# Optimization experiments

Measured on AMD Instinct MI355X. Metric: run time of the kernel, lower is better.

Reference implementation:

```python
import jax, jax.numpy as jnp
import numpy as np

B, S, K = 8, 512, 16  # batch, image size, max highlight points per image
EMPTY_DIST = 362.1    # sentinel used by the torch code when no highlights exist

SOBEL = jnp.array([
    [[[-1.0, 0.0, 1.0], [-2.0, 0.0, 2.0], [-1.0, 0.0, 1.0]]],
    [[[ 1.0, 2.0, 1.0], [ 0.0, 0.0, 0.0], [-1.0, -2.0, -1.0]]],
    [[[ 2.0, 1.0, 0.0], [ 1.0, 0.0, -1.0], [ 0.0, -1.0, -2.0]]],
    [[[ 0.0, 1.0, 2.0], [-1.0, 0.0, 1.0], [-2.0, -1.0, 0.0]]],
], dtype=jnp.float32)  # [4,1,3,3] OIHW


def setup_inputs() -> dict:
    key = jax.random.key(0)
    k1, k2, k3 = jax.random.split(key, 3)
    pred = jax.random.uniform(k1, (B, 1, S, S), dtype=jnp.float32)
    ori_img = jax.random.uniform(k2, (B, 1, S, S), dtype=jnp.float32)
    # sparse point labels: K random highlight pixels per image
    coords = jax.random.randint(k3, (B, K, 2), 0, S)
    b_idx = jnp.repeat(jnp.arange(B), K)
    pt_label = jnp.zeros((B, 1, S, S), dtype=jnp.float32).at[
        b_idx, 0, coords[:, :, 0].reshape(-1), coords[:, :, 1].reshape(-1)
    ].set(1.0)
    return {"pred": pred, "pt_label": pt_label, "ori_img": ori_img}


def _nearest_distance_map(img2d):
    """Per-image exact min Euclidean distance from every pixel to any nonzero pixel.
    Fixed-size (jit-friendly) replacement for nonzero+cdist: top_k finds up to K
    highlight pixels; invalid slots (value==0) are masked with +inf."""
    flat = jnp.abs(img2d).reshape(-1)
    vals, idx = jax.lax.top_k(flat, K)                       # [K]
    ys = (idx // S).astype(jnp.float32)
    xs = (idx % S).astype(jnp.float32)
    gy = jnp.arange(S, dtype=jnp.float32)
    gx = jnp.arange(S, dtype=jnp.float32)
    py = jnp.repeat(gy, S)                                   # [S*S]
    px = jnp.tile(gx, S)
    d = jnp.sqrt((py[:, None] - ys[None, :]) ** 2 + (px[:, None] - xs[None, :]) ** 2)  # [S*S,K]
    valid = vals > 0
    d = jnp.where(valid[None, :], d, jnp.inf)
    dmin = jnp.min(d, axis=1)
    return jnp.where(valid.any(), dmin, EMPTY_DIST).reshape(S, S)


def reference(pred, pt_label, ori_img):
    loss = 1.0
    b, _, s, _ = pred.shape
    distance = jax.vmap(_nearest_distance_map)(pt_label[:, 0])[:, None]  # [B,1,S,S]

    distance_thre = int((1.046 - loss) / 0.046)
    _distance = jnp.where(distance > distance_thre, distance - distance_thre, 0.0)
    _sum = jnp.max(_distance.reshape(b, 1, -1), axis=2)                  # [B,1]
    _distance = _distance / _sum[:, :, None, None]
    distance_loss = jnp.sum(pred * _distance) / (s * s * b)

    img = ori_img * pred
    g = jax.lax.conv_general_dilated(
        img, SOBEL, window_strides=(1, 1), padding=((1, 1), (1, 1)),
        dimension_numbers=("NCHW", "OIHW", "NCHW"))                     # [B,4,S,S]
    g = jnp.max(jnp.abs(g), axis=1, keepdims=True)
    g = g.at[:, :, 0, :].set(0.0).at[:, :, -1, :].set(0.0)
    g = g.at[:, :, :, 0].set(0.0).at[:, :, :, -1].set(0.0)
    gradient_loss = jnp.sum(g) / (s * s * b)
    return (distance_loss, gradient_loss)
```

## Files before the change

### kernel.cpp

```cpp
#include <hip/hip_runtime.h>
#include <math.h>

#define BATCH 8
#define S 512
#define SS (S * S)
#define KMAX 16
#define EMPTY_DD 361.1f
#define SENT 1e9f

#define PTS_OFF  256
#define LSUM_OFF 4352
#define GSUM_OFF 5376
#define LMAX_OFF 6400

__global__ __launch_bounds__(256) void k_points(const float* __restrict__ ptl,
                                                int* __restrict__ wsi) {
    int tid = threadIdx.x;
    int blk = blockIdx.x;
    int b  = blk >> 5;
    int rg = blk & 31;

    __shared__ int l_cnt;
    __shared__ int l_fnd[KMAX];
    if (tid == 0) l_cnt = 0;
    __syncthreads();

    const float4* p4 = (const float4*)(ptl + b * SS + rg * (16 * S));
#pragma unroll
    for (int q = 0; q < 8; q++) {
        float4 v = p4[q * 256 + tid];
        if (v.x + v.y + v.z + v.w != 0.0f) {
            int i0 = rg * (16 * S) + (q * 256 + tid) * 4;
            float c[4] = {v.x, v.y, v.z, v.w};
#pragma unroll
            for (int j = 0; j < 4; j++) {
                if (c[j] != 0.0f) {
                    int slot = atomicAdd(&l_cnt, 1);
                    if (slot < KMAX) l_fnd[slot] = i0 + j;
                }
            }
        }
    }
    __syncthreads();
    int lcnt = l_cnt; if (lcnt > KMAX) lcnt = KMAX;
    if (tid == 0) wsi[blk] = lcnt;
    if (tid < lcnt) wsi[PTS_OFF + blk * KMAX + tid] = l_fnd[tid];
}

__global__ __launch_bounds__(256, 4) void k_main(const float* __restrict__ pred,
                                                 const float* __restrict__ ori,
                                                 const int* __restrict__ wsi,
                                                 float* __restrict__ wsf) {
    int tid = threadIdx.x;
    int blk = blockIdx.x;
    int b  = blk >> 7;
    int rg = blk & 127;
    int wave = tid >> 6;
    int lane = tid & 63;

    __shared__ int l_list[KMAX];
    __shared__ int l_total;
    __shared__ float sm[4][3];

    if (wave == 0) {
        int cj = 0;
        if (lane < 32) cj = wsi[(b << 5) + lane];
        int pre = cj;
#pragma unroll
        for (int d = 1; d < 32; d <<= 1) {
            int t = __shfl_up(pre, d, 64);
            if (lane >= d && lane < 32) pre += t;
        }
        if (lane == 31) l_total = (pre > KMAX) ? KMAX : pre;
        int off = pre - cj;
        if (lane < 32) {
            for (int k = 0; k < cj; k++) {
                if (off + k < KMAX)
                    l_list[off + k] = wsi[PTS_OFF + ((b << 5) + lane) * KMAX + k];
            }
        }
    }
    __syncthreads();

    int cnt = l_total;
    bool has = cnt > 0;
    float pyk[KMAX], pxk[KMAX];
#pragma unroll
    for (int k = 0; k < KMAX; k++) {
        if (k < cnt) {
            int pk = l_list[k];
            pyk[k] = (float)(pk >> 9);
            pxk[k] = (float)(pk & 511);
        } else { pyk[k] = SENT; pxk[k] = SENT; }
    }

    const float* pb = pred + b * SS;
    const float* ob = ori + b * SS;
    int y = rg * 4 + wave;
    int x0 = lane << 3;

    const float4* prow = (const float4*)(pb + y * S + x0);
    float4 pA = prow[0], pB = prow[1];

    float gsum = 0.0f;
    if (y > 0 && y < S - 1) {
        float r[3][10];
#pragma unroll
        for (int ri = 0; ri < 3; ri++) {
            int yy = y - 1 + ri;
            const float4* pr  = (const float4*)(pb + yy * S + x0);
            const float4* orr = (const float4*)(ob + yy * S + x0);
            float4 p0 = (ri == 1) ? pA : pr[0];
            float4 p1 = (ri == 1) ? pB : pr[1];
            float4 o0 = orr[0], o1 = orr[1];
            r[ri][1] = p0.x * o0.x; r[ri][2] = p0.y * o0.y;
            r[ri][3] = p0.z * o0.z; r[ri][4] = p0.w * o0.w;
            r[ri][5] = p1.x * o1.x; r[ri][6] = p1.y * o1.y;
            r[ri][7] = p1.z * o1.z; r[ri][8] = p1.w * o1.w;
            r[ri][0] = __shfl_up(r[ri][8], 1, 64);
            r[ri][9] = __shfl_down(r[ri][1], 1, 64);
        }
#pragma unroll
        for (int j = 0; j < 8; j++) {
            float a00 = r[0][j], a01 = r[0][j + 1], a02 = r[0][j + 2];
            float a10 = r[1][j],                    a12 = r[1][j + 2];
            float a20 = r[2][j], a21 = r[2][j + 1], a22 = r[2][j + 2];
            float g0 = -a00 + a02 - 2.0f * a10 + 2.0f * a12 - a20 + a22;
            float g1 =  a00 + 2.0f * a01 + a02 - a20 - 2.0f * a21 - a22;
            float g2 =  2.0f * a00 + a01 + a10 - a12 - a21 - 2.0f * a22;
            float g3 =  a01 + 2.0f * a02 - a10 + a12 - 2.0f * a20 - a21;
            float gv = fmaxf(fmaxf(fabsf(g0), fabsf(g1)), fmaxf(fabsf(g2), fabsf(g3)));
            bool edge = (lane == 0 && j == 0) || (lane == 63 && j == 7);
            gsum += edge ? 0.0f : gv;
        }
    }

    float fy = (float)y;
    float fx = (float)x0;
    float m[8];
#pragma unroll
    for (int j = 0; j < 8; j++) m[j] = 1e30f;
#pragma unroll
    for (int k = 0; k < KMAX; k++) {
        float dy = fy - pyk[k];
        float dy2 = dy * dy;
        float dx = fx - pxk[k];
#pragma unroll
        for (int j = 0; j < 8; j++) {
            float d = dx + (float)j;
            m[j] = fminf(m[j], fmaf(d, d, dy2));
        }
    }
    float dd[8];
#pragma unroll
    for (int j = 0; j < 8; j++)
        dd[j] = has ? fmaxf(sqrtf(m[j]) - 1.0f, 0.0f) : EMPTY_DD;

    float lsum = pA.x * dd[0] + pA.y * dd[1] + pA.z * dd[2] + pA.w * dd[3] +
                 pB.x * dd[4] + pB.y * dd[5] + pB.z * dd[6] + pB.w * dd[7];
    float lmax = fmaxf(fmaxf(fmaxf(dd[0], dd[1]), fmaxf(dd[2], dd[3])),
                       fmaxf(fmaxf(dd[4], dd[5]), fmaxf(dd[6], dd[7])));

#pragma unroll
    for (int off = 32; off > 0; off >>= 1) {
        lsum += __shfl_down(lsum, off, 64);
        gsum += __shfl_down(gsum, off, 64);
        lmax = fmaxf(lmax, __shfl_down(lmax, off, 64));
    }
    if (lane == 0) { sm[wave][0] = lsum; sm[wave][1] = gsum; sm[wave][2] = lmax; }
    __syncthreads();
    if (tid == 0) {
#pragma unroll
        for (int w = 1; w < 4; w++) {
            lsum += sm[w][0];
            gsum += sm[w][1];
            lmax = fmaxf(lmax, sm[w][2]);
        }
        wsf[LSUM_OFF + blk] = lsum;
        wsf[GSUM_OFF + blk] = gsum;
        wsf[LMAX_OFF + blk] = lmax;
    }
}

__global__ __launch_bounds__(1024) void k_final(const float* __restrict__ wsf,
                                                float* __restrict__ out) {
    int tid = threadIdx.x;
    int lane = tid & 63;
    int w = tid >> 6;

    __shared__ float smf[16][3];

    float ls = wsf[LSUM_OFF + tid];
    float gs = wsf[GSUM_OFF + tid];
    float lm = wsf[LMAX_OFF + tid];
#pragma unroll
    for (int off = 32; off > 0; off >>= 1) {
        ls += __shfl_down(ls, off, 64);
        gs += __shfl_down(gs, off, 64);
        lm = fmaxf(lm, __shfl_down(lm, off, 64));
    }
    if (lane == 0) { smf[w][0] = ls; smf[w][1] = gs; smf[w][2] = lm; }
    __syncthreads();
    if (tid == 0) {
        float dl = 0.0f, gl = 0.0f;
#pragma unroll
        for (int img = 0; img < BATCH; img++) {
            float l = smf[2 * img][0] + smf[2 * img + 1][0];
            float g = smf[2 * img][1] + smf[2 * img + 1][1];
            float mx = fmaxf(smf[2 * img][2], smf[2 * img + 1][2]);
            dl += l / mx;
            gl += g;
        }
        out[0] = dl / (float)(SS * BATCH);
        out[1] = gl / (float)(SS * BATCH);
    }
}

extern "C" void kernel_launch(void* const* d_in, const int* in_sizes, int n_in,
                              void* d_out, int out_size, void* d_ws, size_t ws_size,
                              hipStream_t stream) {
    const float* pred = (const float*)d_in[0];
    const float* ptl  = (const float*)d_in[1];
    const float* ori  = (const float*)d_in[2];
    float* out = (float*)d_out;
    int* wsi = (int*)d_ws;
    float* wsf = (float*)d_ws;

    k_points<<<256, 256, 0, stream>>>(ptl, wsi);
    k_main<<<1024, 256, 0, stream>>>(pred, ori, wsi, wsf);
    k_final<<<1, 1024, 0, stream>>>(wsf, out);
}
```

Baseline: 80.66 us.

## Halve per-thread work and double grid sizes for point scan and main kernel

The point-scan kernel now uses 64 blocks per image of 8 rows each, and the main kernel uses 2048 blocks where each thread handles 4 pixels instead of 8, with each row split across two waves. Halo values at the half-row boundary are loaded directly, and the highlight coordinates are made wave-uniform via readfirstlane so they can sit in scalar registers. The occupancy hint goes from 4 to 8 blocks per CU, and the final reduction reads two partials per thread. The aim is more parallelism and latency hiding, at the cost of more blocks, extra halo loads and more partial results.

```diff
diff --git a/kernel.cpp b/kernel.cpp
--- a/kernel.cpp
+++ b/kernel.cpp
@@ -8,29 +8,29 @@
 #define EMPTY_DD 361.1f
 #define SENT 1e9f
 
-#define PTS_OFF  256
-#define LSUM_OFF 4352
-#define GSUM_OFF 5376
-#define LMAX_OFF 6400
+#define PTS_OFF  512
+#define LSUM_OFF 8704
+#define GSUM_OFF 10752
+#define LMAX_OFF 12800
 
 __global__ __launch_bounds__(256) void k_points(const float* __restrict__ ptl,
                                                 int* __restrict__ wsi) {
     int tid = threadIdx.x;
     int blk = blockIdx.x;
-    int b  = blk >> 5;
-    int rg = blk & 31;
+    int b  = blk >> 6;
+    int rg = blk & 63;
 
     __shared__ int l_cnt;
     __shared__ int l_fnd[KMAX];
     if (tid == 0) l_cnt = 0;
     __syncthreads();
 
-    const float4* p4 = (const float4*)(ptl + b * SS + rg * (16 * S));
-#pragma unroll
-    for (int q = 0; q < 8; q++) {
+    const float4* p4 = (const float4*)(ptl + b * SS + rg * (8 * S));
+#pragma unroll
+    for (int q = 0; q < 4; q++) {
         float4 v = p4[q * 256 + tid];
         if (v.x + v.y + v.z + v.w != 0.0f) {
-            int i0 = rg * (16 * S) + (q * 256 + tid) * 4;
+            int i0 = rg * (8 * S) + (q * 256 + tid) * 4;
             float c[4] = {v.x, v.y, v.z, v.w};
 #pragma unroll
             for (int j = 0; j < 4; j++) {
@@ -47,14 +47,14 @@
     if (tid < lcnt) wsi[PTS_OFF + blk * KMAX + tid] = l_fnd[tid];
 }
 
-__global__ __launch_bounds__(256, 4) void k_main(const float* __restrict__ pred,
+__global__ __launch_bounds__(256, 8) void k_main(const float* __restrict__ pred,
                                                  const float* __restrict__ ori,
                                                  const int* __restrict__ wsi,
                                                  float* __restrict__ wsf) {
     int tid = threadIdx.x;
     int blk = blockIdx.x;
-    int b  = blk >> 7;
-    int rg = blk & 127;
+    int b  = blk >> 8;
+    int rg = blk & 255;
     int wave = tid >> 6;
     int lane = tid & 63;
 
@@ -63,21 +63,18 @@
     __shared__ float sm[4][3];
 
     if (wave == 0) {
-        int cj = 0;
-        if (lane < 32) cj = wsi[(b << 5) + lane];
+        int cj = wsi[(b << 6) + lane];
         int pre = cj;
 #pragma unroll
-        for (int d = 1; d < 32; d <<= 1) {
+        for (int d = 1; d < 64; d <<= 1) {
             int t = __shfl_up(pre, d, 64);
-            if (lane >= d && lane < 32) pre += t;
-        }
-        if (lane == 31) l_total = (pre > KMAX) ? KMAX : pre;
+            if (lane >= d) pre += t;
+        }
+        if (lane == 63) l_total = (pre > KMAX) ? KMAX : pre;
         int off = pre - cj;
-        if (lane < 32) {
-            for (int k = 0; k < cj; k++) {
-                if (off + k < KMAX)
-                    l_list[off + k] = wsi[PTS_OFF + ((b << 5) + lane) * KMAX + k];
-            }
+        for (int k = 0; k < cj; k++) {
+            if (off + k < KMAX)
+                l_list[off + k] = wsi[PTS_OFF + (((b << 6) + lane) << 4) + k];
         }
     }
     __syncthreads();
@@ -87,41 +84,65 @@
     float pyk[KMAX], pxk[KMAX];
 #pragma unroll
     for (int k = 0; k < KMAX; k++) {
-        if (k < cnt) {
-            int pk = l_list[k];
-            pyk[k] = (float)(pk >> 9);
-            pxk[k] = (float)(pk & 511);
-        } else { pyk[k] = SENT; pxk[k] = SENT; }
+        int pk = (k < cnt) ? l_list[k] : -1;
+        float py = (pk >= 0) ? (float)(pk >> 9) : SENT;
+        float px = (pk >= 0) ? (float)(pk & 511) : SENT;
+        pyk[k] = __uint_as_float(__builtin_amdgcn_readfirstlane(__float_as_uint(py)));
+        pxk[k] = __uint_as_float(__builtin_amdgcn_readfirstlane(__float_as_uint(px)));
     }
 
     const float* pb = pred + b * SS;
     const float* ob = ori + b * SS;
-    int y = rg * 4 + wave;
-    int x0 = lane << 3;
-
-    const float4* prow = (const float4*)(pb + y * S + x0);
-    float4 pA = prow[0], pB = prow[1];
+    int y  = (rg << 1) + (wave >> 1);
+    int x0 = ((wave & 1) << 8) | (lane << 2);
+
+    const float4 pA = *(const float4*)(pb + y * S + x0);
+
+    float fy = (float)y;
+    float fx = (float)x0;
+    float m[4];
+#pragma unroll
+    for (int j = 0; j < 4; j++) m[j] = 1e30f;
+#pragma unroll
+    for (int k = 0; k < KMAX; k++) {
+        float dy = fy - pyk[k];
+        float dy2 = dy * dy;
+        float dx = fx - pxk[k];
+#pragma unroll
+        for (int j = 0; j < 4; j++) {
+            float d = dx + (float)j;
+            m[j] = fminf(m[j], fmaf(d, d, dy2));
+        }
+    }
+    float dd[4];
+#pragma unroll
+    for (int j = 0; j < 4; j++)
+        dd[j] = has ? fmaxf(sqrtf(m[j]) - 1.0f, 0.0f) : EMPTY_DD;
+
+    float lsum = pA.x * dd[0] + pA.y * dd[1] + pA.z * dd[2] + pA.w * dd[3];
+    float lmax = fmaxf(fmaxf(dd[0], dd[1]), fmaxf(dd[2], dd[3]));
 
     float gsum = 0.0f;
     if (y > 0 && y < S - 1) {
-        float r[3][10];
+        float r[3][6];
 #pragma unroll
         for (int ri = 0; ri < 3; ri++) {
             int yy = y - 1 + ri;
-            const float4* pr  = (const float4*)(pb + yy * S + x0);
-            const float4* orr = (const float4*)(ob + yy * S + x0);
-            float4 p0 = (ri == 1) ? pA : pr[0];
-            float4 p1 = (ri == 1) ? pB : pr[1];
-            float4 o0 = orr[0], o1 = orr[1];
-            r[ri][1] = p0.x * o0.x; r[ri][2] = p0.y * o0.y;
-            r[ri][3] = p0.z * o0.z; r[ri][4] = p0.w * o0.w;
-            r[ri][5] = p1.x * o1.x; r[ri][6] = p1.y * o1.y;
-            r[ri][7] = p1.z * o1.z; r[ri][8] = p1.w * o1.w;
-            r[ri][0] = __shfl_up(r[ri][8], 1, 64);
-            r[ri][9] = __shfl_down(r[ri][1], 1, 64);
-        }
-#pragma unroll
-        for (int j = 0; j < 8; j++) {
+            const float* prow = pb + yy * S;
+            const float* orow = ob + yy * S;
+            float4 p = (ri == 1) ? pA : *(const float4*)(prow + x0);
+            float4 o = *(const float4*)(orow + x0);
+            float c1 = p.x * o.x, c2 = p.y * o.y, c3 = p.z * o.z, c4 = p.w * o.w;
+            float hl = 0.0f, hr = 0.0f;
+            if (lane == 0 && x0 > 0)        hl = prow[x0 - 1] * orow[x0 - 1];
+            if (lane == 63 && x0 + 4 < S)   hr = prow[x0 + 4] * orow[x0 + 4];
+            float c0 = __shfl_up(c4, 1, 64);   if (lane == 0)  c0 = hl;
+            float c5 = __shfl_down(c1, 1, 64); if (lane == 63) c5 = hr;
+            r[ri][0] = c0; r[ri][1] = c1; r[ri][2] = c2;
+            r[ri][3] = c3; r[ri][4] = c4; r[ri][5] = c5;
+        }
+#pragma unroll
+        for (int j = 0; j < 4; j++) {
             float a00 = r[0][j], a01 = r[0][j + 1], a02 = r[0][j + 2];
             float a10 = r[1][j],                    a12 = r[1][j + 2];
             float a20 = r[2][j], a21 = r[2][j + 1], a22 = r[2][j + 2];
@@ -130,36 +151,10 @@
             float g2 =  2.0f * a00 + a01 + a10 - a12 - a21 - 2.0f * a22;
             float g3 =  a01 + 2.0f * a02 - a10 + a12 - 2.0f * a20 - a21;
             float gv = fmaxf(fmaxf(fabsf(g0), fabsf(g1)), fmaxf(fabsf(g2), fabsf(g3)));
-            bool edge = (lane == 0 && j == 0) || (lane == 63 && j == 7);
-            gsum += edge ? 0.0f : gv;
-        }
-    }
-
-    float fy = (float)y;
-    float fx = (float)x0;
-    float m[8];
-#pragma unroll
-    for (int j = 0; j < 8; j++) m[j] = 1e30f;
-#pragma unroll
-    for (int k = 0; k < KMAX; k++) {
-        float dy = fy - pyk[k];
-        float dy2 = dy * dy;
-        float dx = fx - pxk[k];
-#pragma unroll
-        for (int j = 0; j < 8; j++) {
-            float d = dx + (float)j;
-            m[j] = fminf(m[j], fmaf(d, d, dy2));
-        }
-    }
-    float dd[8];
-#pragma unroll
-    for (int j = 0; j < 8; j++)
-        dd[j] = has ? fmaxf(sqrtf(m[j]) - 1.0f, 0.0f) : EMPTY_DD;
-
-    float lsum = pA.x * dd[0] + pA.y * dd[1] + pA.z * dd[2] + pA.w * dd[3] +
-                 pB.x * dd[4] + pB.y * dd[5] + pB.z * dd[6] + pB.w * dd[7];
-    float lmax = fmaxf(fmaxf(fmaxf(dd[0], dd[1]), fmaxf(dd[2], dd[3])),
-                       fmaxf(fmaxf(dd[4], dd[5]), fmaxf(dd[6], dd[7])));
+            int x = x0 + j;
+            gsum += (x == 0 || x == S - 1) ? 0.0f : gv;
+        }
+    }
 
 #pragma unroll
     for (int off = 32; off > 0; off >>= 1) {
@@ -190,9 +185,10 @@
 
     __shared__ float smf[16][3];
 
-    float ls = wsf[LSUM_OFF + tid];
-    float gs = wsf[GSUM_OFF + tid];
-    float lm = wsf[LMAX_OFF + tid];
+    int i0 = tid << 1;
+    float ls = wsf[LSUM_OFF + i0] + wsf[LSUM_OFF + i0 + 1];
+    float gs = wsf[GSUM_OFF + i0] + wsf[GSUM_OFF + i0 + 1];
+    float lm = fmaxf(wsf[LMAX_OFF + i0], wsf[LMAX_OFF + i0 + 1]);
 #pragma unroll
     for (int off = 32; off > 0; off >>= 1) {
         ls += __shfl_down(ls, off, 64);
@@ -226,7 +222,7 @@
     int* wsi = (int*)d_ws;
     float* wsf = (float*)d_ws;
 
-    k_points<<<256, 256, 0, stream>>>(ptl, wsi);
-    k_main<<<1024, 256, 0, stream>>>(pred, ori, wsi, wsf);
+    k_points<<<512, 256, 0, stream>>>(ptl, wsi);
+    k_main<<<2048, 256, 0, stream>>>(pred, ori, wsi, wsf);
     k_final<<<1, 1024, 0, stream>>>(wsf, out);
 }
```

Result: slower. 84.26 us (+4.5%).

## Hoist stencil loads before point gather and rebalance grid sizes

Applied to the files above, without the earlier changes.

The stencil loads of pred and ori for all three rows are now issued before the wave-0 point-list gather and the barrier, so global memory latency overlaps the prefix scan. The distance loop is moved ahead of the Sobel compute. k_points is split into 1024 blocks of 4 rows each for more parallelism during the scan. k_main uses 512 blocks of 512 threads (8 rows per block), which changes the workspace offsets and the final reduction. The trade-offs are higher register pressure from holding the loaded rows across the barrier and a longer 128-entry prefix scan per block.

```diff
diff --git a/kernel.cpp b/kernel.cpp
--- a/kernel.cpp
+++ b/kernel.cpp
@@ -8,29 +8,29 @@
 #define EMPTY_DD 361.1f
 #define SENT 1e9f
 
-#define PTS_OFF  256
-#define LSUM_OFF 4352
-#define GSUM_OFF 5376
-#define LMAX_OFF 6400
+#define PTS_OFF  1024
+#define LSUM_OFF 17408
+#define GSUM_OFF 17920
+#define LMAX_OFF 18432
 
 __global__ __launch_bounds__(256) void k_points(const float* __restrict__ ptl,
                                                 int* __restrict__ wsi) {
     int tid = threadIdx.x;
     int blk = blockIdx.x;
-    int b  = blk >> 5;
-    int rg = blk & 31;
+    int b  = blk >> 7;
+    int rg = blk & 127;
 
     __shared__ int l_cnt;
     __shared__ int l_fnd[KMAX];
     if (tid == 0) l_cnt = 0;
     __syncthreads();
 
-    const float4* p4 = (const float4*)(ptl + b * SS + rg * (16 * S));
-#pragma unroll
-    for (int q = 0; q < 8; q++) {
+    const float4* p4 = (const float4*)(ptl + b * SS + rg * (4 * S));
+#pragma unroll
+    for (int q = 0; q < 2; q++) {
         float4 v = p4[q * 256 + tid];
         if (v.x + v.y + v.z + v.w != 0.0f) {
-            int i0 = rg * (16 * S) + (q * 256 + tid) * 4;
+            int i0 = rg * (4 * S) + (q * 256 + tid) * 4;
             float c[4] = {v.x, v.y, v.z, v.w};
 #pragma unroll
             for (int j = 0; j < 4; j++) {
@@ -47,38 +47,79 @@
     if (tid < lcnt) wsi[PTS_OFF + blk * KMAX + tid] = l_fnd[tid];
 }
 
-__global__ __launch_bounds__(256, 4) void k_main(const float* __restrict__ pred,
+__global__ __launch_bounds__(512, 4) void k_main(const float* __restrict__ pred,
                                                  const float* __restrict__ ori,
                                                  const int* __restrict__ wsi,
                                                  float* __restrict__ wsf) {
     int tid = threadIdx.x;
     int blk = blockIdx.x;
-    int b  = blk >> 7;
-    int rg = blk & 127;
+    int b  = blk >> 6;
+    int rg = blk & 63;
     int wave = tid >> 6;
     int lane = tid & 63;
 
     __shared__ int l_list[KMAX];
     __shared__ int l_total;
-    __shared__ float sm[4][3];
+    __shared__ float sm[8][3];
+
+    const float* pb = pred + b * SS;
+    const float* ob = ori + b * SS;
+    int y  = (rg << 3) + wave;
+    int x0 = lane << 3;
+
+    const float4* pc = (const float4*)(pb + y * S + x0);
+    float4 pA = pc[0], pB = pc[1];
+
+    bool inner = (y > 0 && y < S - 1);
+    float r[3][10];
+    if (inner) {
+        const float4* pu = (const float4*)(pb + (y - 1) * S + x0);
+        const float4* pd = (const float4*)(pb + (y + 1) * S + x0);
+        const float4* ou = (const float4*)(ob + (y - 1) * S + x0);
+        const float4* om = (const float4*)(ob + y * S + x0);
+        const float4* od = (const float4*)(ob + (y + 1) * S + x0);
+        float4 pu0 = pu[0], pu1 = pu[1], pd0 = pd[0], pd1 = pd[1];
+        float4 ou0 = ou[0], ou1 = ou[1], om0 = om[0], om1 = om[1];
+        float4 od0 = od[0], od1 = od[1];
+        r[0][1] = pu0.x * ou0.x; r[0][2] = pu0.y * ou0.y;
+        r[0][3] = pu0.z * ou0.z; r[0][4] = pu0.w * ou0.w;
+        r[0][5] = pu1.x * ou1.x; r[0][6] = pu1.y * ou1.y;
+        r[0][7] = pu1.z * ou1.z; r[0][8] = pu1.w * ou1.w;
+        r[1][1] = pA.x * om0.x;  r[1][2] = pA.y * om0.y;
+        r[1][3] = pA.z * om0.z;  r[1][4] = pA.w * om0.w;
+        r[1][5] = pB.x * om1.x;  r[1][6] = pB.y * om1.y;
+        r[1][7] = pB.z * om1.z;  r[1][8] = pB.w * om1.w;
+        r[2][1] = pd0.x * od0.x; r[2][2] = pd0.y * od0.y;
+        r[2][3] = pd0.z * od0.z; r[2][4] = pd0.w * od0.w;
+        r[2][5] = pd1.x * od1.x; r[2][6] = pd1.y * od1.y;
+        r[2][7] = pd1.z * od1.z; r[2][8] = pd1.w * od1.w;
+#pragma unroll
+        for (int ri = 0; ri < 3; ri++) {
+            r[ri][0] = __shfl_up(r[ri][8], 1, 64);
+            r[ri][9] = __shfl_down(r[ri][1], 1, 64);
+        }
+    }
 
     if (wave == 0) {
-        int cj = 0;
-        if (lane < 32) cj = wsi[(b << 5) + lane];
-        int pre = cj;
-#pragma unroll
-        for (int d = 1; d < 32; d <<= 1) {
-            int t = __shfl_up(pre, d, 64);
-            if (lane >= d && lane < 32) pre += t;
-        }
-        if (lane == 31) l_total = (pre > KMAX) ? KMAX : pre;
-        int off = pre - cj;
-        if (lane < 32) {
-            for (int k = 0; k < cj; k++) {
-                if (off + k < KMAX)
-                    l_list[off + k] = wsi[PTS_OFF + ((b << 5) + lane) * KMAX + k];
-            }
-        }
+        int base = b << 7;
+        int cj0 = wsi[base + 2 * lane];
+        int cj1 = wsi[base + 2 * lane + 1];
+        int ps = cj0 + cj1;
+        int incl = ps;
+#pragma unroll
+        for (int d = 1; d < 64; d <<= 1) {
+            int t = __shfl_up(incl, d, 64);
+            if (lane >= d) incl += t;
+        }
+        if (lane == 63) l_total = (incl > KMAX) ? KMAX : incl;
+        int excl = incl - ps;
+        int off0 = excl, off1 = excl + cj0;
+        for (int k = 0; k < cj0; k++)
+            if (off0 + k < KMAX)
+                l_list[off0 + k] = wsi[PTS_OFF + (base + 2 * lane) * KMAX + k];
+        for (int k = 0; k < cj1; k++)
+            if (off1 + k < KMAX)
+                l_list[off1 + k] = wsi[PTS_OFF + (base + 2 * lane + 1) * KMAX + k];
     }
     __syncthreads();
 
@@ -94,32 +135,34 @@
         } else { pyk[k] = SENT; pxk[k] = SENT; }
     }
 
-    const float* pb = pred + b * SS;
-    const float* ob = ori + b * SS;
-    int y = rg * 4 + wave;
-    int x0 = lane << 3;
-
-    const float4* prow = (const float4*)(pb + y * S + x0);
-    float4 pA = prow[0], pB = prow[1];
+    float fy = (float)y;
+    float fx = (float)x0;
+    float m[8];
+#pragma unroll
+    for (int j = 0; j < 8; j++) m[j] = 1e30f;
+#pragma unroll
+    for (int k = 0; k < KMAX; k++) {
+        float dy = fy - pyk[k];
+        float dy2 = dy * dy;
+        float dx = fx - pxk[k];
+#pragma unroll
+        for (int j = 0; j < 8; j++) {
+            float d = dx + (float)j;
+            m[j] = fminf(m[j], fmaf(d, d, dy2));
+        }
+    }
+    float dd[8];
+#pragma unroll
+    for (int j = 0; j < 8; j++)
+        dd[j] = has ? fmaxf(sqrtf(m[j]) - 1.0f, 0.0f) : EMPTY_DD;
+
+    float lsum = pA.x * dd[0] + pA.y * dd[1] + pA.z * dd[2] + pA.w * dd[3] +
+                 pB.x * dd[4] + pB.y * dd[5] + pB.z * dd[6] + pB.w * dd[7];
+    float lmax = fmaxf(fmaxf(fmaxf(dd[0], dd[1]), fmaxf(dd[2], dd[3])),
+                       fmaxf(fmaxf(dd[4], dd[5]), fmaxf(dd[6], dd[7])));
 
     float gsum = 0.0f;
-    if (y > 0 && y < S - 1) {
-        float r[3][10];
-#pragma unroll
-        for (int ri = 0; ri < 3; ri++) {
-            int yy = y - 1 + ri;
-            const float4* pr  = (const float4*)(pb + yy * S + x0);
-            const float4* orr = (const float4*)(ob + yy * S + x0);
-            float4 p0 = (ri == 1) ? pA : pr[0];
-            float4 p1 = (ri == 1) ? pB : pr[1];
-            float4 o0 = orr[0], o1 = orr[1];
-            r[ri][1] = p0.x * o0.x; r[ri][2] = p0.y * o0.y;
-            r[ri][3] = p0.z * o0.z; r[ri][4] = p0.w * o0.w;
-            r[ri][5] = p1.x * o1.x; r[ri][6] = p1.y * o1.y;
-            r[ri][7] = p1.z * o1.z; r[ri][8] = p1.w * o1.w;
-            r[ri][0] = __shfl_up(r[ri][8], 1, 64);
-            r[ri][9] = __shfl_down(r[ri][1], 1, 64);
-        }
+    if (inner) {
 #pragma unroll
         for (int j = 0; j < 8; j++) {
             float a00 = r[0][j], a01 = r[0][j + 1], a02 = r[0][j + 2];
@@ -135,32 +178,6 @@
         }
     }
 
-    float fy = (float)y;
-    float fx = (float)x0;
-    float m[8];
-#pragma unroll
-    for (int j = 0; j < 8; j++) m[j] = 1e30f;
-#pragma unroll
-    for (int k = 0; k < KMAX; k++) {
-        float dy = fy - pyk[k];
-        float dy2 = dy * dy;
-        float dx = fx - pxk[k];
-#pragma unroll
-        for (int j = 0; j < 8; j++) {
-            float d = dx + (float)j;
-            m[j] = fminf(m[j], fmaf(d, d, dy2));
-        }
-    }
-    float dd[8];
-#pragma unroll
-    for (int j = 0; j < 8; j++)
-        dd[j] = has ? fmaxf(sqrtf(m[j]) - 1.0f, 0.0f) : EMPTY_DD;
-
-    float lsum = pA.x * dd[0] + pA.y * dd[1] + pA.z * dd[2] + pA.w * dd[3] +
-                 pB.x * dd[4] + pB.y * dd[5] + pB.z * dd[6] + pB.w * dd[7];
-    float lmax = fmaxf(fmaxf(fmaxf(dd[0], dd[1]), fmaxf(dd[2], dd[3])),
-                       fmaxf(fmaxf(dd[4], dd[5]), fmaxf(dd[6], dd[7])));
-
 #pragma unroll
     for (int off = 32; off > 0; off >>= 1) {
         lsum += __shfl_down(lsum, off, 64);
@@ -171,7 +188,7 @@
     __syncthreads();
     if (tid == 0) {
 #pragma unroll
-        for (int w = 1; w < 4; w++) {
+        for (int w = 1; w < 8; w++) {
             lsum += sm[w][0];
             gsum += sm[w][1];
             lmax = fmaxf(lmax, sm[w][2]);
@@ -182,17 +199,18 @@
     }
 }
 
-__global__ __launch_bounds__(1024) void k_final(const float* __restrict__ wsf,
-                                                float* __restrict__ out) {
+__global__ __launch_bounds__(512) void k_final(const float* __restrict__ wsf,
+                                               float* __restrict__ out) {
     int tid = threadIdx.x;
     int lane = tid & 63;
     int w = tid >> 6;
 
-    __shared__ float smf[16][3];
-
-    float ls = wsf[LSUM_OFF + tid];
-    float gs = wsf[GSUM_OFF + tid];
-    float lm = wsf[LMAX_OFF + tid];
+    __shared__ float smf[8][3];
+
+    int idx = (w << 6) + lane;
+    float ls = wsf[LSUM_OFF + idx];
+    float gs = wsf[GSUM_OFF + idx];
+    float lm = wsf[LMAX_OFF + idx];
 #pragma unroll
     for (int off = 32; off > 0; off >>= 1) {
         ls += __shfl_down(ls, off, 64);
@@ -205,11 +223,8 @@
         float dl = 0.0f, gl = 0.0f;
 #pragma unroll
         for (int img = 0; img < BATCH; img++) {
-            float l = smf[2 * img][0] + smf[2 * img + 1][0];
-            float g = smf[2 * img][1] + smf[2 * img + 1][1];
-            float mx = fmaxf(smf[2 * img][2], smf[2 * img + 1][2]);
-            dl += l / mx;
-            gl += g;
+            dl += smf[img][0] / smf[img][2];
+            gl += smf[img][1];
         }
         out[0] = dl / (float)(SS * BATCH);
         out[1] = gl / (float)(SS * BATCH);
@@ -226,7 +241,7 @@
     int* wsi = (int*)d_ws;
     float* wsf = (float*)d_ws;
 
-    k_points<<<256, 256, 0, stream>>>(ptl, wsi);
-    k_main<<<1024, 256, 0, stream>>>(pred, ori, wsi, wsf);
-    k_final<<<1, 1024, 0, stream>>>(wsf, out);
-}
+    k_points<<<1024, 256, 0, stream>>>(ptl, wsi);
+    k_main<<<512, 512, 0, stream>>>(pred, ori, wsi, wsf);
+    k_final<<<1, 512, 0, stream>>>(wsf, out);
+}
```

After: 82.44 us. +2.2%, slower.
